# Kernel tuning notes

Measured on AMD Instinct MI355X. Metric: run time of the kernel, lower is better.

## Reference

```python
import jax, jax.numpy as jnp
import numpy as np

N, E, F_IN, F_OUT = 16384, 4096, 128, 128
EPS = 1e-6


def setup_inputs() -> dict:
    key = jax.random.key(0)
    k1, k2, k3 = jax.random.split(key, 3)
    H = (jax.random.uniform(k1, (N, E)) < 0.05).astype(jnp.float32)
    x = jax.random.normal(k2, (N, F_IN), dtype=jnp.float32)
    W = jax.random.normal(k3, (F_IN, F_OUT), dtype=jnp.float32) * 0.05
    return {"x": x, "H": H, "W": W}


def reference(x, H, W):
    # D_v^{-1} H D_e^{-1} H^T x W, computed without materializing the NxN
    # adjacency: diagonal matmuls become row/col broadcast scaling, and the
    # GEMM chain is reordered right-to-left (same math, associativity).
    d_e_inv = 1.0 / (H.sum(axis=0) + EPS)   # [E]
    d_v_inv = 1.0 / (H.sum(axis=1) + EPS)   # [N]
    xw = x @ W                               # [N, F_out]
    edge_msg = H.T @ xw                      # [E, F_out] gather onto edges
    edge_msg = d_e_inv[:, None] * edge_msg   # D_e^{-1}
    node_msg = H @ edge_msg                  # [N, F_out] scatter back to nodes
    return d_v_inv[:, None] * node_msg       # D_v^{-1}
```

## Files before the change

kernel.cpp:

```cpp
#include <hip/hip_runtime.h>
#include <stdint.h>

#define N_NODES 16384
#define N_EDGES 4096
#define FDIM    128
#define EPSF    1e-6f

typedef __attribute__((ext_vector_type(8))) short short8;
typedef __attribute__((ext_vector_type(4))) float f32x4;

__device__ __forceinline__ unsigned short f2bf(float f) {
    uint32_t u = __float_as_uint(f);
    return (unsigned short)((u + 0x7FFFu + ((u >> 16) & 1u)) >> 16);
}

__global__ __launch_bounds__(256) void k_bitpack(const float* __restrict__ H,
        unsigned long long* __restrict__ bitsNE, float* __restrict__ dvinv) {
    int w = threadIdx.x >> 6, lane = threadIdx.x & 63;
    int n = blockIdx.x * 4 + w;
    const float* hr = H + (size_t)n * N_EDGES;
    unsigned long long* out = bitsNE + (size_t)n * (N_EDGES / 64);
    int cnt = 0;
    for (int c = 0; c < N_EDGES / 64; ++c) {
        float v = hr[c * 64 + lane];
        unsigned long long m = __ballot(v > 0.5f);
        cnt += __popcll(m);
        if (lane == 0) out[c] = m;
    }
    if (lane == 0) dvinv[n] = 1.0f / ((float)cnt + EPSF);
}

__global__ __launch_bounds__(256) void k_transpose(const unsigned long long* __restrict__ bitsNE,
        unsigned long long* __restrict__ bitsEN) {
    int w = threadIdx.x >> 6, lane = threadIdx.x & 63;
    int wid = blockIdx.x * 4 + w;
    int et = wid & 63, nt = wid >> 6;
    unsigned long long q = bitsNE[(size_t)(nt * 64 + lane) * (N_EDGES / 64) + et];
    unsigned long long outv = 0;
    for (int j = 0; j < 64; ++j) {
        unsigned long long r = __ballot((int)((q >> j) & 1ULL));
        if (lane == j) outv = r;
    }
    bitsEN[(size_t)(et * 64 + lane) * (N_NODES / 64) + nt] = outv;
}

__global__ __launch_bounds__(256) void k_edeg(const unsigned long long* __restrict__ bitsEN,
        float* __restrict__ deinv) {
    int w = threadIdx.x >> 6, lane = threadIdx.x & 63;
    int e = blockIdx.x * 4 + w;
    const unsigned long long* r = bitsEN + (size_t)e * (N_NODES / 64);
    int s = __popcll(r[lane]) + __popcll(r[lane + 64]) + __popcll(r[lane + 128]) + __popcll(r[lane + 192]);
    for (int o = 32; o; o >>= 1) s += __shfl_xor(s, o);
    if (lane == 0) deinv[e] = 1.0f / ((float)s + EPSF);
}

__global__ __launch_bounds__(256) void k_xw(const float* __restrict__ x, const float* __restrict__ W,
        unsigned short* __restrict__ xwT) {
    __shared__ __attribute__((aligned(16))) unsigned short ldsWT[128 * 136];
    __shared__ __attribute__((aligned(16))) unsigned short ldsT[128 * 72];
    int t = threadIdx.x, lane = t & 63, w = t >> 6;
    int r16 = lane & 15, klane = lane >> 4;
    for (int i = 0; i < 64; ++i) {
        int idx = i * 256 + t;
        int k = idx >> 7, f = idx & 127;
        ldsWT[f * 136 + k] = f2bf(W[idx]);
    }
    __syncthreads();
    int nbase = blockIdx.x * 64;
    int row = nbase + w * 16 + r16;
    const float* xr = x + (size_t)row * FDIM;
    f32x4 acc[8] = {};
    for (int kb = 0; kb < 128; kb += 32) {
        union { short8 v; unsigned short u[8]; } a;
        #pragma unroll
        for (int j = 0; j < 8; ++j) a.u[j] = f2bf(xr[kb + klane * 8 + j]);
        #pragma unroll
        for (int fb = 0; fb < 8; ++fb) {
            short8 b = *(const short8*)&ldsWT[(fb * 16 + r16) * 136 + kb + klane * 8];
            acc[fb] = __builtin_amdgcn_mfma_f32_16x16x32_bf16(a.v, b, acc[fb], 0, 0, 0);
        }
    }
    #pragma unroll
    for (int fb = 0; fb < 8; ++fb)
        #pragma unroll
        for (int r = 0; r < 4; ++r)
            ldsT[(fb * 16 + r16) * 72 + w * 16 + klane * 4 + r] = f2bf(acc[fb][r]);
    __syncthreads();
    int f = t >> 1, part = t & 1;
    #pragma unroll
    for (int j = 0; j < 4; ++j)
        *(uint4*)&xwT[(size_t)f * N_NODES + nbase + part * 32 + j * 8] =
            *(const uint4*)&ldsT[f * 72 + part * 32 + j * 8];
}

template<bool FINAL>
__global__ __launch_bounds__(256) void k_gemm_bits(
        const unsigned long long* __restrict__ bits, int krows ,
        const unsigned short* __restrict__ BT, int K,
        float* __restrict__ Cout, const float* __restrict__ rowScale,
        int M, int pairs) {
    __shared__ __attribute__((aligned(16))) unsigned short ldsB[128 * 72];
    int t = threadIdx.x, lane = t & 63, w = t >> 6;
    int r16 = lane & 15, klane = lane >> 4;
    int fh = (w & 1) * 64;
    int mbase = blockIdx.x * 32 + (w >> 1) * 16;
    int kq0 = blockIdx.z * pairs;
    const unsigned long long* brow = bits + (size_t)(mbase + r16) * krows + kq0;
    int srow = t >> 1, shalf = t & 1;
    const unsigned short* sBT = BT + (size_t)srow * K + shalf * 32;
    unsigned short* sL = ldsB + srow * 72 + shalf * 32;
    f32x4 acc[4] = {};
    for (int p = 0; p < pairs; ++p) {
        int kb = (kq0 + p) * 64;
        const unsigned short* src = sBT + kb;
        uint4 v0 = *(const uint4*)(src);
        uint4 v1 = *(const uint4*)(src + 8);
        uint4 v2 = *(const uint4*)(src + 16);
        uint4 v3 = *(const uint4*)(src + 24);
        unsigned long long q = brow[p];
        *(uint4*)(sL) = v0; *(uint4*)(sL + 8) = v1;
        *(uint4*)(sL + 16) = v2; *(uint4*)(sL + 24) = v3;
        __syncthreads();
        #pragma unroll
        for (int s = 0; s < 2; ++s) {
            uint32_t b8 = (uint32_t)(q >> (s * 32 + klane * 8)) & 0xFFu;
            union { short8 v; uint32_t u[4]; } a;
            a.u[0] = ((b8 & 1u)  ? 0x3F80u : 0u) | ((b8 & 2u)   ? 0x3F800000u : 0u);
            a.u[1] = ((b8 & 4u)  ? 0x3F80u : 0u) | ((b8 & 8u)   ? 0x3F800000u : 0u);
            a.u[2] = ((b8 & 16u) ? 0x3F80u : 0u) | ((b8 & 32u)  ? 0x3F800000u : 0u);
            a.u[3] = ((b8 & 64u) ? 0x3F80u : 0u) | ((b8 & 128u) ? 0x3F800000u : 0u);
            #pragma unroll
            for (int fb = 0; fb < 4; ++fb) {
                short8 b = *(const short8*)&ldsB[(fh + fb * 16 + r16) * 72 + s * 32 + klane * 8];
                acc[fb] = __builtin_amdgcn_mfma_f32_16x16x32_bf16(a.v, b, acc[fb], 0, 0, 0);
            }
        }
        __syncthreads();
    }
    if (FINAL) {
        #pragma unroll
        for (int fb = 0; fb < 4; ++fb)
            #pragma unroll
            for (int r = 0; r < 4; ++r) {
                int row = mbase + klane * 4 + r;
                Cout[(size_t)row * FDIM + fh + fb * 16 + r16] = rowScale[row] * acc[fb][r];
            }
    } else {
        float* P = Cout + (size_t)blockIdx.z * M * FDIM;
        #pragma unroll
        for (int fb = 0; fb < 4; ++fb)
            #pragma unroll
            for (int r = 0; r < 4; ++r) {
                int row = mbase + klane * 4 + r;
                P[(size_t)row * FDIM + fh + fb * 16 + r16] = acc[fb][r];
            }
    }
}

__global__ __launch_bounds__(256) void k_reduce_scale_T(const float* __restrict__ partials,
        const float* __restrict__ deinv, unsigned short* __restrict__ emT, int S) {
    __shared__ float lds[64 * 129];
    int t = threadIdx.x;
    int e0 = blockIdx.x * 64;
    for (int i = 0; i < 32; ++i) {
        int idx = i * 256 + t;
        int e_l = idx >> 7, f = idx & 127;
        float s = 0.f;
        for (int z = 0; z < S; ++z)
            s += partials[(size_t)z * N_EDGES * FDIM + (size_t)(e0 + e_l) * FDIM + f];
        lds[e_l * 129 + f] = s * deinv[e0 + e_l];
    }
    __syncthreads();
    for (int i = 0; i < 32; ++i) {
        int idx = i * 256 + t;
        int f = idx >> 6, e_l = idx & 63;
        emT[(size_t)f * N_EDGES + e0 + e_l] = f2bf(lds[e_l * 129 + f]);
    }
}

extern "C" void kernel_launch(void* const* d_in, const int* in_sizes, int n_in,
                              void* d_out, int out_size, void* d_ws, size_t ws_size,
                              hipStream_t stream) {
    const float* x = (const float*)d_in[0];
    const float* H = (const float*)d_in[1];
    const float* W = (const float*)d_in[2];
    float* out = (float*)d_out;
    char* ws = (char*)d_ws;

    unsigned long long* bitsNE = (unsigned long long*)(ws);
    unsigned long long* bitsEN = (unsigned long long*)(ws + (8u << 20));
    unsigned short* xwT = (unsigned short*)(ws + (16u << 20));
    unsigned short* emT = (unsigned short*)(ws + (20u << 20));
    float* dvinv = (float*)(ws + (21u << 20));
    float* deinv = (float*)(ws + (21u << 20) + 65536);
    size_t pbase = (21u << 20) + 65536 + 16384;
    float* partials = (float*)(ws + pbase);

    int S = 8;
    while (S > 1 && pbase + (size_t)S * N_EDGES * FDIM * 4 > ws_size) S >>= 1;

    hipLaunchKernelGGL(k_bitpack, dim3(4096), dim3(256), 0, stream, H, bitsNE, dvinv);
    hipLaunchKernelGGL(k_transpose, dim3(4096), dim3(256), 0, stream, bitsNE, bitsEN);
    hipLaunchKernelGGL(k_edeg, dim3(1024), dim3(256), 0, stream, bitsEN, deinv);
    hipLaunchKernelGGL(k_xw, dim3(256), dim3(256), 0, stream, x, W, xwT);
    hipLaunchKernelGGL((k_gemm_bits<false>), dim3(128, 1, S), dim3(256), 0, stream,
                       bitsEN, N_NODES / 64, xwT, N_NODES, partials, (const float*)nullptr,
                       N_EDGES, (N_NODES / 64) / S);
    hipLaunchKernelGGL(k_reduce_scale_T, dim3(64), dim3(256), 0, stream, partials, deinv, emT, S);
    hipLaunchKernelGGL((k_gemm_bits<true>), dim3(512, 1, 1), dim3(256), 0, stream,
                       bitsNE, N_EDGES / 64, emT, N_EDGES, out, dvinv,
                       N_NODES, N_EDGES / 64);
}
```

Baseline: 294.7 us.

## Permute bit/K layouts so GEMM loads B directly from global with register double-buffering

```diff
diff --git a/kernel.cpp b/kernel.cpp
--- a/kernel.cpp
+++ b/kernel.cpp
@@ -8,54 +8,91 @@
 
 typedef __attribute__((ext_vector_type(8))) short short8;
 typedef __attribute__((ext_vector_type(4))) float f32x4;
+typedef unsigned long long ull;
 
 __device__ __forceinline__ unsigned short f2bf(float f) {
     uint32_t u = __float_as_uint(f);
     return (unsigned short)((u + 0x7FFFu + ((u >> 16) & 1u)) >> 16);
 }
 
+__device__ __forceinline__ short8 as_s8(uint4 v) {
+    union { uint4 a; short8 b; } u; u.a = v; return u.b;
+}
+
+__device__ __forceinline__ short8 expand8(uint32_t half, int bitoff) {
+    uint32_t b8 = (half >> bitoff) & 0xFFu;
+    uint32_t lo = ((b8 & 0xFu) * 0x00204081u) & 0x01010101u;
+    uint32_t hi = ((b8 >> 4) * 0x00204081u) & 0x01010101u;
+    union { short8 v; uint32_t u[4]; } a;
+#if __has_builtin(__builtin_amdgcn_perm)
+    a.u[0] = __builtin_amdgcn_perm(0u, lo, 0x04010400u) * 0x3F80u;
+    a.u[1] = __builtin_amdgcn_perm(0u, lo, 0x04030402u) * 0x3F80u;
+    a.u[2] = __builtin_amdgcn_perm(0u, hi, 0x04010400u) * 0x3F80u;
+    a.u[3] = __builtin_amdgcn_perm(0u, hi, 0x04030402u) * 0x3F80u;
+#else
+    a.u[0] = ((lo & 1u)         | ((lo >> 8) & 1u) << 16) * 0x3F80u;
+    a.u[1] = (((lo >> 16) & 1u) | ((lo >> 24) & 1u) << 16) * 0x3F80u;
+    a.u[2] = ((hi & 1u)         | ((hi >> 8) & 1u) << 16) * 0x3F80u;
+    a.u[3] = (((hi >> 16) & 1u) | ((hi >> 24) & 1u) << 16) * 0x3F80u;
+#endif
+    return a.v;
+}
+
 __global__ __launch_bounds__(256) void k_bitpack(const float* __restrict__ H,
-        unsigned long long* __restrict__ bitsNE, float* __restrict__ dvinv) {
+        ull* __restrict__ bitsNE, float* __restrict__ dvinv) {
     int w = threadIdx.x >> 6, lane = threadIdx.x & 63;
     int n = blockIdx.x * 4 + w;
-    const float* hr = H + (size_t)n * N_EDGES;
-    unsigned long long* out = bitsNE + (size_t)n * (N_EDGES / 64);
+    const float4* hr = (const float4*)(H + (size_t)n * N_EDGES);
+    ull* out = bitsNE + (size_t)n * (N_EDGES / 64);
     int cnt = 0;
-    for (int c = 0; c < N_EDGES / 64; ++c) {
-        float v = hr[c * 64 + lane];
-        unsigned long long m = __ballot(v > 0.5f);
-        cnt += __popcll(m);
-        if (lane == 0) out[c] = m;
+    for (int c4 = 0; c4 < N_EDGES / 256; ++c4) {
+        float4 v = hr[c4 * 64 + lane];
+        ull b0 = __ballot(v.x > 0.5f);
+        ull b1 = __ballot(v.y > 0.5f);
+        ull b2 = __ballot(v.z > 0.5f);
+        ull b3 = __ballot(v.w > 0.5f);
+        cnt += __popcll(b0) + __popcll(b1) + __popcll(b2) + __popcll(b3);
+        if (lane == 0) {
+            #pragma unroll
+            for (int q = 0; q < 4; ++q) {
+                ull wq = ((b0 >> (16 * q)) & 0xFFFFull)
+                       | (((b1 >> (16 * q)) & 0xFFFFull) << 16)
+                       | (((b2 >> (16 * q)) & 0xFFFFull) << 32)
+                       | (((b3 >> (16 * q)) & 0xFFFFull) << 48);
+                out[c4 * 4 + q] = wq;
+            }
+        }
     }
     if (lane == 0) dvinv[n] = 1.0f / ((float)cnt + EPSF);
 }
 
-__global__ __launch_bounds__(256) void k_transpose(const unsigned long long* __restrict__ bitsNE,
-        unsigned long long* __restrict__ bitsEN) {
+__global__ __launch_bounds__(256) void k_transpose(const ull* __restrict__ bitsNE,
+        ull* __restrict__ bitsEN) {
     int w = threadIdx.x >> 6, lane = threadIdx.x & 63;
     int wid = blockIdx.x * 4 + w;
     int et = wid & 63, nt = wid >> 6;
-    unsigned long long q = bitsNE[(size_t)(nt * 64 + lane) * (N_EDGES / 64) + et];
-    unsigned long long outv = 0;
+    int pl = 4 * (lane & 15) + (lane >> 4);
+    ull q = bitsNE[(size_t)(nt * 64 + pl) * (N_EDGES / 64) + et];
+    ull outv = 0;
     for (int j = 0; j < 64; ++j) {
-        unsigned long long r = __ballot((int)((q >> j) & 1ULL));
+        ull r = __ballot((int)((q >> j) & 1ULL));
         if (lane == j) outv = r;
     }
-    bitsEN[(size_t)(et * 64 + lane) * (N_NODES / 64) + nt] = outv;
-}
-
-__global__ __launch_bounds__(256) void k_edeg(const unsigned long long* __restrict__ bitsEN,
+    bitsEN[(size_t)(et * 64 + pl) * (N_NODES / 64) + nt] = outv;
+}
+
+__global__ __launch_bounds__(256) void k_edeg(const ull* __restrict__ bitsEN,
         float* __restrict__ deinv) {
     int w = threadIdx.x >> 6, lane = threadIdx.x & 63;
     int e = blockIdx.x * 4 + w;
-    const unsigned long long* r = bitsEN + (size_t)e * (N_NODES / 64);
+    const ull* r = bitsEN + (size_t)e * (N_NODES / 64);
     int s = __popcll(r[lane]) + __popcll(r[lane + 64]) + __popcll(r[lane + 128]) + __popcll(r[lane + 192]);
     for (int o = 32; o; o >>= 1) s += __shfl_xor(s, o);
     if (lane == 0) deinv[e] = 1.0f / ((float)s + EPSF);
 }
 
 __global__ __launch_bounds__(256) void k_xw(const float* __restrict__ x, const float* __restrict__ W,
-        unsigned short* __restrict__ xwT) {
+        unsigned short* __restrict__ xwTp) {
     __shared__ __attribute__((aligned(16))) unsigned short ldsWT[128 * 136];
     __shared__ __attribute__((aligned(16))) unsigned short ldsT[128 * 72];
     int t = threadIdx.x, lane = t & 63, w = t >> 6;
@@ -68,12 +105,14 @@
     __syncthreads();
     int nbase = blockIdx.x * 64;
     int row = nbase + w * 16 + r16;
-    const float* xr = x + (size_t)row * FDIM;
+    const float4* xr4 = (const float4*)(x + (size_t)row * FDIM);
     f32x4 acc[8] = {};
     for (int kb = 0; kb < 128; kb += 32) {
+        float4 u0 = xr4[(kb >> 2) + klane * 2];
+        float4 u1 = xr4[(kb >> 2) + klane * 2 + 1];
         union { short8 v; unsigned short u[8]; } a;
-        #pragma unroll
-        for (int j = 0; j < 8; ++j) a.u[j] = f2bf(xr[kb + klane * 8 + j]);
+        a.u[0] = f2bf(u0.x); a.u[1] = f2bf(u0.y); a.u[2] = f2bf(u0.z); a.u[3] = f2bf(u0.w);
+        a.u[4] = f2bf(u1.x); a.u[5] = f2bf(u1.y); a.u[6] = f2bf(u1.z); a.u[7] = f2bf(u1.w);
         #pragma unroll
         for (int fb = 0; fb < 8; ++fb) {
             short8 b = *(const short8*)&ldsWT[(fb * 16 + r16) * 136 + kb + klane * 8];
@@ -84,81 +123,85 @@
     for (int fb = 0; fb < 8; ++fb)
         #pragma unroll
         for (int r = 0; r < 4; ++r)
-            ldsT[(fb * 16 + r16) * 72 + w * 16 + klane * 4 + r] = f2bf(acc[fb][r]);
+            ldsT[(fb * 16 + r16) * 72 + 16 * r + w * 4 + klane] = f2bf(acc[fb][r]);
     __syncthreads();
     int f = t >> 1, part = t & 1;
     #pragma unroll
     for (int j = 0; j < 4; ++j)
-        *(uint4*)&xwT[(size_t)f * N_NODES + nbase + part * 32 + j * 8] =
+        *(uint4*)&xwTp[(size_t)f * N_NODES + nbase + part * 32 + j * 8] =
             *(const uint4*)&ldsT[f * 72 + part * 32 + j * 8];
 }
+
+#define LOADP(Q0, Q1, BUF, p) do { \
+    Q0 = brow0[(p)]; Q1 = brow1[(p)]; \
+    const unsigned short* _src = bcol + (size_t)(p) * 64; \
+    _Pragma("unroll") \
+    for (int _fb = 0; _fb < 4; ++_fb) { \
+        BUF[_fb * 2]     = *(const uint4*)(_src + _fb * fbstride); \
+        BUF[_fb * 2 + 1] = *(const uint4*)(_src + _fb * fbstride + 32); \
+    } } while (0)
+
+#define COMPUTEP(Q0, Q1, BUF) do { \
+    _Pragma("unroll") \
+    for (int _s = 0; _s < 2; ++_s) { \
+        uint32_t _h0 = (uint32_t)(_s == 0 ? (Q0) : ((Q0) >> 32)); \
+        uint32_t _h1 = (uint32_t)(_s == 0 ? (Q1) : ((Q1) >> 32)); \
+        short8 _a0 = expand8(_h0, bitoff); \
+        short8 _a1 = expand8(_h1, bitoff); \
+        _Pragma("unroll") \
+        for (int _fb = 0; _fb < 4; ++_fb) { \
+            short8 _b = as_s8(BUF[_fb * 2 + _s]); \
+            acc[0][_fb] = __builtin_amdgcn_mfma_f32_16x16x32_bf16(_a0, _b, acc[0][_fb], 0, 0, 0); \
+            acc[1][_fb] = __builtin_amdgcn_mfma_f32_16x16x32_bf16(_a1, _b, acc[1][_fb], 0, 0, 0); \
+        } } } while (0)
 
 template<bool FINAL>
 __global__ __launch_bounds__(256) void k_gemm_bits(
-        const unsigned long long* __restrict__ bits, int krows ,
+        const ull* __restrict__ bits, int krows,
         const unsigned short* __restrict__ BT, int K,
         float* __restrict__ Cout, const float* __restrict__ rowScale,
         int M, int pairs) {
-    __shared__ __attribute__((aligned(16))) unsigned short ldsB[128 * 72];
     int t = threadIdx.x, lane = t & 63, w = t >> 6;
     int r16 = lane & 15, klane = lane >> 4;
-    int fh = (w & 1) * 64;
-    int mbase = blockIdx.x * 32 + (w >> 1) * 16;
-    int kq0 = blockIdx.z * pairs;
-    const unsigned long long* brow = bits + (size_t)(mbase + r16) * krows + kq0;
-    int srow = t >> 1, shalf = t & 1;
-    const unsigned short* sBT = BT + (size_t)srow * K + shalf * 32;
-    unsigned short* sL = ldsB + srow * 72 + shalf * 32;
-    f32x4 acc[4] = {};
-    for (int p = 0; p < pairs; ++p) {
-        int kb = (kq0 + p) * 64;
-        const unsigned short* src = sBT + kb;
-        uint4 v0 = *(const uint4*)(src);
-        uint4 v1 = *(const uint4*)(src + 8);
-        uint4 v2 = *(const uint4*)(src + 16);
-        uint4 v3 = *(const uint4*)(src + 24);
-        unsigned long long q = brow[p];
-        *(uint4*)(sL) = v0; *(uint4*)(sL + 8) = v1;
-        *(uint4*)(sL + 16) = v2; *(uint4*)(sL + 24) = v3;
-        __syncthreads();
-        #pragma unroll
-        for (int s = 0; s < 2; ++s) {
-            uint32_t b8 = (uint32_t)(q >> (s * 32 + klane * 8)) & 0xFFu;
-            union { short8 v; uint32_t u[4]; } a;
-            a.u[0] = ((b8 & 1u)  ? 0x3F80u : 0u) | ((b8 & 2u)   ? 0x3F800000u : 0u);
-            a.u[1] = ((b8 & 4u)  ? 0x3F80u : 0u) | ((b8 & 8u)   ? 0x3F800000u : 0u);
-            a.u[2] = ((b8 & 16u) ? 0x3F80u : 0u) | ((b8 & 32u)  ? 0x3F800000u : 0u);
-            a.u[3] = ((b8 & 64u) ? 0x3F80u : 0u) | ((b8 & 128u) ? 0x3F800000u : 0u);
-            #pragma unroll
-            for (int fb = 0; fb < 4; ++fb) {
-                short8 b = *(const short8*)&ldsB[(fh + fb * 16 + r16) * 72 + s * 32 + klane * 8];
-                acc[fb] = __builtin_amdgcn_mfma_f32_16x16x32_bf16(a.v, b, acc[fb], 0, 0, 0);
-            }
-        }
-        __syncthreads();
-    }
-    if (FINAL) {
+    int bitoff = klane * 8;
+    int wm = w >> 1, wf = w & 1;
+    int mbase = blockIdx.x * 64 + wm * 32;
+    int kw0 = blockIdx.z * pairs;
+    const ull* brow0 = bits + (size_t)(mbase + r16) * krows + kw0;
+    const ull* brow1 = brow0 + (size_t)16 * krows;
+    const unsigned short* bcol = BT + (size_t)(wf * 64 + r16) * K + (size_t)kw0 * 64 + klane * 8;
+    const int fbstride = 16 * K;
+
+    f32x4 acc[2][4] = {};
+    ull qA0, qA1, qB0, qB1;
+    uint4 bufA[8], bufB[8];
+
+    LOADP(qA0, qA1, bufA, 0);
+    for (int p = 0; p < pairs; p += 2) {
+        LOADP(qB0, qB1, bufB, p + 1);
+        COMPUTEP(qA0, qA1, bufA);
+        if (p + 2 < pairs) LOADP(qA0, qA1, bufA, p + 2);
+        COMPUTEP(qB0, qB1, bufB);
+    }
+
+    #pragma unroll
+    for (int fr = 0; fr < 2; ++fr)
         #pragma unroll
         for (int fb = 0; fb < 4; ++fb)
             #pragma unroll
             for (int r = 0; r < 4; ++r) {
-                int row = mbase + klane * 4 + r;
-                Cout[(size_t)row * FDIM + fh + fb * 16 + r16] = rowScale[row] * acc[fb][r];
+                int row = mbase + fr * 16 + klane * 4 + r;
+                int col = wf * 64 + fb * 16 + r16;
+                float v = acc[fr][fb][r];
+                if (FINAL)
+                    Cout[(size_t)row * FDIM + col] = rowScale[row] * v;
+                else
+                    Cout[(size_t)blockIdx.z * M * FDIM + (size_t)row * FDIM + col] = v;
             }
-    } else {
-        float* P = Cout + (size_t)blockIdx.z * M * FDIM;
-        #pragma unroll
-        for (int fb = 0; fb < 4; ++fb)
-            #pragma unroll
-            for (int r = 0; r < 4; ++r) {
-                int row = mbase + klane * 4 + r;
-                P[(size_t)row * FDIM + fh + fb * 16 + r16] = acc[fb][r];
-            }
-    }
 }
 
 __global__ __launch_bounds__(256) void k_reduce_scale_T(const float* __restrict__ partials,
-        const float* __restrict__ deinv, unsigned short* __restrict__ emT, int S) {
+        const float* __restrict__ deinv, unsigned short* __restrict__ emTp, int S) {
     __shared__ float lds[64 * 129];
     int t = threadIdx.x;
     int e0 = blockIdx.x * 64;
@@ -173,8 +216,9 @@
     __syncthreads();
     for (int i = 0; i < 32; ++i) {
         int idx = i * 256 + t;
-        int f = idx >> 6, e_l = idx & 63;
-        emT[(size_t)f * N_EDGES + e0 + e_l] = f2bf(lds[e_l * 129 + f]);
+        int f = idx >> 6, j = idx & 63;
+        int pj = 4 * (j & 15) + (j >> 4);
+        emTp[(size_t)f * N_EDGES + e0 + j] = f2bf(lds[pj * 129 + f]);
     }
 }
 
@@ -187,27 +231,27 @@
     float* out = (float*)d_out;
     char* ws = (char*)d_ws;
 
-    unsigned long long* bitsNE = (unsigned long long*)(ws);
-    unsigned long long* bitsEN = (unsigned long long*)(ws + (8u << 20));
-    unsigned short* xwT = (unsigned short*)(ws + (16u << 20));
-    unsigned short* emT = (unsigned short*)(ws + (20u << 20));
+    ull* bitsNE = (ull*)(ws);
+    ull* bitsEN = (ull*)(ws + (8u << 20));
+    unsigned short* xwTp = (unsigned short*)(ws + (16u << 20));
+    unsigned short* emTp = (unsigned short*)(ws + (20u << 20));
     float* dvinv = (float*)(ws + (21u << 20));
     float* deinv = (float*)(ws + (21u << 20) + 65536);
     size_t pbase = (21u << 20) + 65536 + 16384;
     float* partials = (float*)(ws + pbase);
 
-    int S = 8;
+    int S = 4;
     while (S > 1 && pbase + (size_t)S * N_EDGES * FDIM * 4 > ws_size) S >>= 1;
 
     hipLaunchKernelGGL(k_bitpack, dim3(4096), dim3(256), 0, stream, H, bitsNE, dvinv);
     hipLaunchKernelGGL(k_transpose, dim3(4096), dim3(256), 0, stream, bitsNE, bitsEN);
     hipLaunchKernelGGL(k_edeg, dim3(1024), dim3(256), 0, stream, bitsEN, deinv);
-    hipLaunchKernelGGL(k_xw, dim3(256), dim3(256), 0, stream, x, W, xwT);
-    hipLaunchKernelGGL((k_gemm_bits<false>), dim3(128, 1, S), dim3(256), 0, stream,
-                       bitsEN, N_NODES / 64, xwT, N_NODES, partials, (const float*)nullptr,
+    hipLaunchKernelGGL(k_xw, dim3(256), dim3(256), 0, stream, x, W, xwTp);
+    hipLaunchKernelGGL((k_gemm_bits<false>), dim3(64, 1, S), dim3(256), 0, stream,
+                       bitsEN, N_NODES / 64, xwTp, N_NODES, partials, (const float*)nullptr,
                        N_EDGES, (N_NODES / 64) / S);
-    hipLaunchKernelGGL(k_reduce_scale_T, dim3(64), dim3(256), 0, stream, partials, deinv, emT, S);
-    hipLaunchKernelGGL((k_gemm_bits<true>), dim3(512, 1, 1), dim3(256), 0, stream,
-                       bitsNE, N_EDGES / 64, emT, N_EDGES, out, dvinv,
+    hipLaunchKernelGGL(k_reduce_scale_T, dim3(64), dim3(256), 0, stream, partials, deinv, emTp, S);
+    hipLaunchKernelGGL((k_gemm_bits<true>), dim3(256, 1, 1), dim3(256), 0, stream,
+                       bitsNE, N_EDGES / 64, emTp, N_EDGES, out, dvinv,
                        N_NODES, N_EDGES / 64);
 }
```

After: 264.6 us. 10.2% less time.
